# Performance work log

Hardware: AMD Instinct MI355X
Metric: run time of the kernel (lower is better)

The kernel has to match this reference:

```python
import jax, jax.numpy as jnp
import numpy as np

B, N, A = 4096, 16, 8          # envs, num_agents, num_actions
D_IN, H1, DP, DZ = 128, 64, 64, 64  # obs dim, gnn hidden, obs_proc dim, gat fc dim


def _init(k, shape):
    return jax.random.normal(k, shape, jnp.float32) / np.sqrt(shape[0]).astype(np.float32)


def setup_inputs() -> dict:
    key = jax.random.key(0)
    ks = jax.random.split(key, 8)
    return {
        "obs": jax.random.normal(ks[0], (B * N, D_IN), jnp.float32),
        "policies": jax.random.uniform(ks[1], (B * N, A), dtype=jnp.float32),
        "actions": jax.random.uniform(ks[2], (B * N, A), dtype=jnp.float32),
        "W1": _init(ks[3], (D_IN, H1)), "b1": jnp.zeros((H1,), jnp.float32),
        "W2": _init(ks[4], (H1, DP)), "b2": jnp.zeros((DP,), jnp.float32),
        "Wfc": _init(ks[5], (DP, DZ)),
        "Wattn": _init(ks[6], (2 * DZ, 1)),
        "Wv": _init(ks[7], (DP + A, 1)), "bv": jnp.zeros((1,), jnp.float32),
    }


def reference(obs, policies, actions, W1, b1, W2, b2, Wfc, Wattn, Wv, bv):
    obs = obs.reshape(B, N, D_IN)
    # --- CriticInputPreprocess: two mean-aggregation GNN layers on a complete
    # graph with self-loops -> every node sees the per-env mean.
    agg1 = jnp.mean(obs, axis=1)                      # [B, D_IN]
    h = jax.nn.relu(agg1 @ W1 + b1)                   # [B, H1] (identical across nodes)
    obs_proc1 = h @ W2 + b2                           # mean of identical features is itself
    obs_proc = jnp.broadcast_to(obs_proc1[:, None, :], (B, N, DP))  # [B, N, DP]
    # --- GATLayer edge attention: e_{d<-s} = leaky_relu(attn([z_s, z_d]))
    z_ = obs_proc @ Wfc                               # [B, N, DZ]
    a_src = (z_ @ Wattn[:DZ]).squeeze(-1)             # [B, N]
    a_dst = (z_ @ Wattn[DZ:]).squeeze(-1)             # [B, N]
    e = jax.nn.leaky_relu(a_src[:, None, :] + a_dst[:, :, None])    # [B, dst, src]
    w = jax.nn.sigmoid(e)                             # [B, N, N]
    pi = policies.reshape(B, N, A)
    act = actions.reshape(B, N, A)
    # mailbox mix per (dst d, src k): z = w*act_k + (1-w)*pi_k
    z = w[..., None] * act[:, None, :, :] + (1.0 - w[..., None]) * pi[:, None, :, :]  # [B,d,k,A]
    # place_policies/place_zs + mean over src axis collapses to:
    # y[b,d,j] = (pi[b,j] + sum_{k!=j} z[b,d,k]) / N
    y = (jnp.sum(z, axis=2, keepdims=True) - z + pi[:, None, :, :]) / N               # [B,d,j,A]
    obs_rep = jnp.broadcast_to(obs_proc[:, None, :, :], (B, N, N, DP))                # obs_proc[b, j]
    obs_final = jnp.concatenate([obs_rep, y], axis=-1).reshape(B * N, N, DP + A)
    x = obs_final @ Wv + bv                           # [B*N, N, 1]
    return x, w.reshape(B * N, N, 1)
```

## Files before the change

### kernel.cpp

```cpp
#include <hip/hip_runtime.h>

#define BB   4096
#define NN   16
#define AA   8
#define DIN  128
#define H1C  64
#define DPC  64
#define DZC  64

#define GENV 8
#define NTHR 512


__device__ __forceinline__ float lane_bcast(float v, int lane) {
    return __int_as_float(__builtin_amdgcn_readlane(__float_as_int(v), lane));
}

__global__ __launch_bounds__(NTHR, 4)
void critic_kernel(const float* __restrict__ obs,
                   const float* __restrict__ policies,
                   const float* __restrict__ actions,
                   const float* __restrict__ W1,
                   const float* __restrict__ b1,
                   const float* __restrict__ W2,
                   const float* __restrict__ b2,
                   const float* __restrict__ Wfc,
                   const float* __restrict__ Wattn,
                   const float* __restrict__ Wv,
                   const float* __restrict__ bv,
                   float* __restrict__ out_x,
                   float* __restrict__ out_w)
{
    __shared__ float4 sW1T4[H1C * 32];
    __shared__ float sV1[H1C];
    __shared__ float sV2[H1C];
    __shared__ float sS[2];
    __shared__ float sDv[GENV][16];
    __shared__ float sWsum[DZC];
    __shared__ float sWv64[DPC];
    __shared__ float sU[DPC];

    const int tid = threadIdx.x;
    const int l   = tid & 63;
    const int w   = tid >> 6;
    const int e   = blockIdx.x * GENV + w;

    {
        const int c   = tid & 63;
        const int grp = tid >> 6;
        #pragma unroll
        for (int i = 0; i < 4; ++i) {
            const int d0 = 4 * (i * 8 + grp);
            const float w0  = W1[(d0 + 0) * H1C + c];
            const float w1_ = W1[(d0 + 1) * H1C + c];
            const float w2_ = W1[(d0 + 2) * H1C + c];
            const float w3_ = W1[(d0 + 3) * H1C + c];
            sW1T4[c * 32 + ((d0 >> 2) ^ (c & 7))] = make_float4(w0, w1_, w2_, w3_);
        }
    }

    const float2* o2p = reinterpret_cast<const float2*>(obs) + (size_t)e * (NN * DIN / 2);
    float2 ov[NN];
    #pragma unroll
    for (int r = 0; r < NN; ++r) ov[r] = o2p[r * 64 + l];

    const float* Pb = policies + (size_t)e * (NN * AA);
    const float* Ab = actions  + (size_t)e * (NN * AA);
    const float pv0 = Pb[l], pv1 = Pb[64 + l];
    const float av0 = Ab[l], av1 = Ab[64 + l];

    const float b1v = b1[l];
    const float va  = Wv[64 + (l & 7)];
    const float bvv = bv[0];

    if (w == 7) {
        const float b2v  = b2[l];
        const float wsum = Wattn[l] + Wattn[DZC + l];
        const float wvv  = Wv[l];
        sWsum[l] = wsum;
        sWv64[l] = wvv;

        float u = 0.0f;
        {
            const float4* WfcR = reinterpret_cast<const float4*>(Wfc) + (size_t)l * (DZC / 4);
            const float4* ws4  = reinterpret_cast<const float4*>(sWsum);
            #pragma unroll
            for (int j4 = 0; j4 < DZC / 4; ++j4) {
                const float4 wq = WfcR[j4];
                const float4 s  = ws4[j4];
                u = fmaf(wq.x, s.x, u); u = fmaf(wq.y, s.y, u);
                u = fmaf(wq.z, s.z, u); u = fmaf(wq.w, s.w, u);
            }
        }
        sU[l] = u;
        float v1 = 0.0f, v2 = 0.0f;
        {
            const float4* W2R = reinterpret_cast<const float4*>(W2) + (size_t)l * (DPC / 4);
            const float4* su4 = reinterpret_cast<const float4*>(sU);
            const float4* sv4 = reinterpret_cast<const float4*>(sWv64);
            #pragma unroll
            for (int j4 = 0; j4 < DPC / 4; ++j4) {
                const float4 wq = W2R[j4];
                const float4 a  = su4[j4];
                const float4 b  = sv4[j4];
                v1 = fmaf(wq.x, a.x, v1); v1 = fmaf(wq.y, a.y, v1);
                v1 = fmaf(wq.z, a.z, v1); v1 = fmaf(wq.w, a.w, v1);
                v2 = fmaf(wq.x, b.x, v2); v2 = fmaf(wq.y, b.y, v2);
                v2 = fmaf(wq.z, b.z, v2); v2 = fmaf(wq.w, b.w, v2);
            }
        }
        float tb2u = b2v * u;
        float tb2w = b2v * wvv;
        #pragma unroll
        for (int m = 32; m >= 1; m >>= 1) {
            tb2u += __shfl_xor(tb2u, m);
            tb2w += __shfl_xor(tb2w, m);
        }
        sV1[l] = v1;
        sV2[l] = v2;
        if (l == 0) { sS[0] = tb2u; sS[1] = tb2w; }
    }

    float ax, ay;
    {
        float sx = 0.0f, sy = 0.0f;
        #pragma unroll
        for (int r = 0; r < NN; ++r) { sx += ov[r].x; sy += ov[r].y; }
        const float inv = 1.0f / 16.0f;
        ax = sx * inv;
        ay = sy * inv;
    }

    float q0 = (pv0 - av0) * va;
    float q1 = (pv1 - av1) * va;
    float fq = q0 + q1;
    float fp = (pv0 + pv1) * va;
    #pragma unroll
    for (int m = 1; m <= 4; m <<= 1) {
        q0 += __shfl_xor(q0, m);
        q1 += __shfl_xor(q1, m);
    }
    #pragma unroll
    for (int m = 32; m >= 1; m >>= 1) {
        fq += __shfl_xor(fq, m);
        fp += __shfl_xor(fp, m);
    }
    if ((l & 7) == 0) {
        sDv[w][l >> 3]       = q0;
        sDv[w][8 + (l >> 3)] = q1;
    }

    __syncthreads();

    float a0 = b1v, a1 = 0.0f, a2 = 0.0f, a3 = 0.0f;
    #pragma unroll
    for (int d4 = 0; d4 < DIN / 4; ++d4) {
        const float4 w4 = sW1T4[l * 32 + (d4 ^ (l & 7))];
        a0 = fmaf(lane_bcast(ax, 2 * d4),     w4.x, a0);
        a1 = fmaf(lane_bcast(ay, 2 * d4),     w4.y, a1);
        a2 = fmaf(lane_bcast(ax, 2 * d4 + 1), w4.z, a2);
        a3 = fmaf(lane_bcast(ay, 2 * d4 + 1), w4.w, a3);
    }
    const float h = fmaxf((a0 + a1) + (a2 + a3), 0.0f);

    const float v1l  = sV1[l];
    const float v2l  = sV2[l];
    const float tb2u = sS[0];
    const float tb2w = sS[1];

    float t0 = h * v1l;
    float t1 = h * v2l;
    #pragma unroll
    for (int m = 32; m >= 1; m >>= 1) {
        t0 += __shfl_xor(t0, m);
        t1 += __shfl_xor(t1, m);
    }
    const float logit = t0 + tb2u;
    const float eV  = (logit > 0.0f) ? logit : 0.01f * logit;
    const float wgt = 1.0f / (1.0f + expf(-eV));
    const float c   = t1 + tb2w + bvv;
    const float Sv  = fp - wgt * fq;

    const float invN = 1.0f / 16.0f;
    const int j0 = (4 * l) & 15;
    float4 xo, wo;
    xo.x = fmaf(wgt, sDv[w][j0 + 0], Sv) * invN + c;
    xo.y = fmaf(wgt, sDv[w][j0 + 1], Sv) * invN + c;
    xo.z = fmaf(wgt, sDv[w][j0 + 2], Sv) * invN + c;
    xo.w = fmaf(wgt, sDv[w][j0 + 3], Sv) * invN + c;
    wo.x = wo.y = wo.z = wo.w = wgt;

    const size_t base = (size_t)e * (NN * NN) + 4 * l;
    *reinterpret_cast<float4*>(out_x + base) = xo;
    *reinterpret_cast<float4*>(out_w + base) = wo;
}

extern "C" void kernel_launch(void* const* d_in, const int* in_sizes, int n_in,
                              void* d_out, int out_size, void* d_ws, size_t ws_size,
                              hipStream_t stream) {
    const float* obs      = (const float*)d_in[0];
    const float* policies = (const float*)d_in[1];
    const float* actions  = (const float*)d_in[2];
    const float* W1       = (const float*)d_in[3];
    const float* b1       = (const float*)d_in[4];
    const float* W2       = (const float*)d_in[5];
    const float* b2       = (const float*)d_in[6];
    const float* Wfc      = (const float*)d_in[7];
    const float* Wattn    = (const float*)d_in[8];
    const float* Wv       = (const float*)d_in[9];
    const float* bv       = (const float*)d_in[10];

    float* out_x = (float*)d_out;
    float* out_w = out_x + (size_t)BB * NN * NN;

    critic_kernel<<<BB / GENV, NTHR, 0, stream>>>(obs, policies, actions,
                                                  W1, b1, W2, b2, Wfc, Wattn, Wv, bv,
                                                  out_x, out_w);
}
```

Before: 17.42 us.

## Split obs mean aggregation into a separate pre-kernel writing to workspace

Moves the per-environment mean over the 16 agents' observations into its own kernel with smaller blocks, which writes the aggregated vectors to workspace. The main critic kernel then reads only the 128-float aggregate per environment instead of the full observation tile. The aim is to lower register pressure and latency in the main kernel and let the obs streaming run at higher occupancy. The cost is an extra launch and a workspace write-then-read round trip.

```diff
diff --git a/kernel.cpp b/kernel.cpp
--- a/kernel.cpp
+++ b/kernel.cpp
@@ -16,8 +16,29 @@
     return __int_as_float(__builtin_amdgcn_readlane(__float_as_int(v), lane));
 }
 
+__global__ __launch_bounds__(256, 4)
+void agg_kernel(const float* __restrict__ obs,
+                float* __restrict__ agg)
+{
+    const int tid = threadIdx.x;
+    const int l   = tid & 63;
+    const int w   = tid >> 6;
+    const int e   = blockIdx.x * 4 + w;
+
+    const float2* o2 = reinterpret_cast<const float2*>(obs) + (size_t)e * (NN * DIN / 2);
+    float2 ov[NN];
+    #pragma unroll
+    for (int r = 0; r < NN; ++r) ov[r] = o2[r * 64 + l];
+
+    float sx = 0.0f, sy = 0.0f;
+    #pragma unroll
+    for (int r = 0; r < NN; ++r) { sx += ov[r].x; sy += ov[r].y; }
+    const float inv = 1.0f / 16.0f;
+    reinterpret_cast<float2*>(agg)[(size_t)e * 64 + l] = make_float2(sx * inv, sy * inv);
+}
+
 __global__ __launch_bounds__(NTHR, 4)
-void critic_kernel(const float* __restrict__ obs,
+void critic_kernel(const float* __restrict__ agg,
                    const float* __restrict__ policies,
                    const float* __restrict__ actions,
                    const float* __restrict__ W1,
@@ -45,6 +66,9 @@
     const int w   = tid >> 6;
     const int e   = blockIdx.x * GENV + w;
 
+    const float2 agv = reinterpret_cast<const float2*>(agg)[(size_t)e * 64 + l];
+    const float ax = agv.x, ay = agv.y;
+
     {
         const int c   = tid & 63;
         const int grp = tid >> 6;
@@ -58,11 +82,6 @@
             sW1T4[c * 32 + ((d0 >> 2) ^ (c & 7))] = make_float4(w0, w1_, w2_, w3_);
         }
     }
-
-    const float2* o2p = reinterpret_cast<const float2*>(obs) + (size_t)e * (NN * DIN / 2);
-    float2 ov[NN];
-    #pragma unroll
-    for (int r = 0; r < NN; ++r) ov[r] = o2p[r * 64 + l];
 
     const float* Pb = policies + (size_t)e * (NN * AA);
     const float* Ab = actions  + (size_t)e * (NN * AA);
@@ -109,45 +128,30 @@
                 v2 = fmaf(wq.z, b.z, v2); v2 = fmaf(wq.w, b.w, v2);
             }
         }
-        float tb2u = b2v * u;
-        float tb2w = b2v * wvv;
+        float tb2u_ = b2v * u;
+        float tb2w_ = b2v * wvv;
         #pragma unroll
         for (int m = 32; m >= 1; m >>= 1) {
-            tb2u += __shfl_xor(tb2u, m);
-            tb2w += __shfl_xor(tb2w, m);
+            tb2u_ += __shfl_xor(tb2u_, m);
+            tb2w_ += __shfl_xor(tb2w_, m);
         }
         sV1[l] = v1;
         sV2[l] = v2;
-        if (l == 0) { sS[0] = tb2u; sS[1] = tb2w; }
-    }
-
-    float ax, ay;
+        if (l == 0) { sS[0] = tb2u_; sS[1] = tb2w_; }
+    }
+
+    float fqv, fpv;
     {
-        float sx = 0.0f, sy = 0.0f;
-        #pragma unroll
-        for (int r = 0; r < NN; ++r) { sx += ov[r].x; sy += ov[r].y; }
-        const float inv = 1.0f / 16.0f;
-        ax = sx * inv;
-        ay = sy * inv;
-    }
-
-    float q0 = (pv0 - av0) * va;
-    float q1 = (pv1 - av1) * va;
-    float fq = q0 + q1;
-    float fp = (pv0 + pv1) * va;
-    #pragma unroll
-    for (int m = 1; m <= 4; m <<= 1) {
-        q0 += __shfl_xor(q0, m);
-        q1 += __shfl_xor(q1, m);
-    }
-    #pragma unroll
-    for (int m = 32; m >= 1; m >>= 1) {
-        fq += __shfl_xor(fq, m);
-        fp += __shfl_xor(fp, m);
-    }
-    if ((l & 7) == 0) {
-        sDv[w][l >> 3]       = q0;
-        sDv[w][8 + (l >> 3)] = q1;
+        float q0 = (pv0 - av0) * va;
+        float q1 = (pv1 - av1) * va;
+        float fq = q0 + q1;
+        float fp = (pv0 + pv1) * va;
+        #pragma unroll
+        for (int m = 1; m <= 4; m <<= 1) { q0 += __shfl_xor(q0, m); q1 += __shfl_xor(q1, m); }
+        #pragma unroll
+        for (int m = 32; m >= 1; m >>= 1) { fq += __shfl_xor(fq, m); fp += __shfl_xor(fp, m); }
+        fqv = fq; fpv = fp;
+        if ((l & 7) == 0) { sDv[w][l >> 3] = q0; sDv[w][8 + (l >> 3)] = q1; }
     }
 
     __syncthreads();
@@ -179,7 +183,7 @@
     const float eV  = (logit > 0.0f) ? logit : 0.01f * logit;
     const float wgt = 1.0f / (1.0f + expf(-eV));
     const float c   = t1 + tb2w + bvv;
-    const float Sv  = fp - wgt * fq;
+    const float Sv  = fpv - wgt * fqv;
 
     const float invN = 1.0f / 16.0f;
     const int j0 = (4 * l) & 15;
@@ -212,8 +216,10 @@
 
     float* out_x = (float*)d_out;
     float* out_w = out_x + (size_t)BB * NN * NN;
-
-    critic_kernel<<<BB / GENV, NTHR, 0, stream>>>(obs, policies, actions,
+    float* agg   = (float*)d_ws;
+
+    agg_kernel<<<BB / 4, 256, 0, stream>>>(obs, agg);
+    critic_kernel<<<BB / GENV, NTHR, 0, stream>>>(agg, policies, actions,
                                                   W1, b1, W2, b2, Wfc, Wattn, Wv, bv,
                                                   out_x, out_w);
 }
```

After: 20.40 us. 1.17x slower.
